# Kernel tuning notes

Measured on AMD Instinct MI355X. Metric: run time of the kernel, lower is better.

The kernel has to match this reference:

```python
import jax, jax.numpy as jnp
import numpy as np

N = 100000
E = 1600000
R = 8
DIN = 128
H = 128
C = 16
NROOT = 1024


def rgcn_conv(x, src, dst, edge_type, w_rel, w_root, bias):
    """PyG RGCNConv: per-relation mean aggregation + root weight + bias."""
    n, din = x.shape
    r = w_rel.shape[0]
    msgs = x[src]  # [E, din] gather
    seg = dst * r + edge_type  # combined (node, relation) segment id
    sums = jax.ops.segment_sum(msgs, seg, num_segments=n * r)        # [N*R, din]
    cnt = jax.ops.segment_sum(jnp.ones((msgs.shape[0],), x.dtype), seg,
                              num_segments=n * r)                    # [N*R]
    mean = sums / jnp.maximum(cnt, 1.0)[:, None]
    mean = mean.reshape(n, r, din)
    # relation-specific transform then sum over relations, plus root transform
    out = jnp.einsum('nrd,rde->ne', mean, w_rel) + x @ w_root + bias
    return out


def setup_inputs() -> dict:
    key = jax.random.key(0)
    ks = jax.random.split(key, 16)
    s = 0.05
    return {
        'x': jax.random.normal(ks[0], (N, DIN), jnp.float32),
        'edge_index': jax.random.randint(ks[1], (2, E), 0, N, jnp.int64),
        'edge_type': jax.random.randint(ks[2], (E,), 0, R, jnp.int64),
        'root_idx': jax.random.randint(ks[3], (NROOT,), 0, N, jnp.int64),
        'wrel1': jax.random.normal(ks[4], (R, DIN, H), jnp.float32) * s,
        'root1': jax.random.normal(ks[5], (DIN, H), jnp.float32) * s,
        'b1': jax.random.normal(ks[6], (H,), jnp.float32) * s,
        'wrel2': jax.random.normal(ks[7], (R, H, H), jnp.float32) * s,
        'root2': jax.random.normal(ks[8], (H, H), jnp.float32) * s,
        'b2': jax.random.normal(ks[9], (H,), jnp.float32) * s,
        'wrel3': jax.random.normal(ks[10], (R, H, C), jnp.float32) * s,
        'root3': jax.random.normal(ks[11], (H, C), jnp.float32) * s,
        'b3': jax.random.normal(ks[12], (C,), jnp.float32) * s,
    }


def reference(x, edge_index, edge_type, root_idx,
              wrel1, root1, b1, wrel2, root2, b2, wrel3, root3, b3):
    src, dst = edge_index[0], edge_index[1]
    h = jax.nn.relu(rgcn_conv(x, src, dst, edge_type, wrel1, root1, b1))
    # hidden conv (relu; dropout is identity in eval mode)
    h = jax.nn.relu(rgcn_conv(h, src, dst, edge_type, wrel2, root2, b2))
    # final conv, no activation
    h = rgcn_conv(h, src, dst, edge_type, wrel3, root3, b3)
    return h[root_idx]  # [NROOT, C]
```

## Files before the change

kernel.cpp:

```cpp
#include <hip/hip_runtime.h>
#include <hip/hip_fp16.h>


typedef _Float16 f16;
typedef _Float16 f16x2 __attribute__((ext_vector_type(2)));
typedef _Float16 f16x4 __attribute__((ext_vector_type(4)));
typedef _Float16 f16x8 __attribute__((ext_vector_type(8)));
typedef float f32x4 __attribute__((ext_vector_type(4)));

#define NREL 8
#define ACHUNK 8192

__global__ void k_hist(const int* __restrict__ dst, int E, int* __restrict__ cnt) {
  int e = blockIdx.x * 256 + threadIdx.x;
  if (e < E) atomicAdd(&cnt[dst[e]], 1);
}

__global__ void k_scan1(const int* __restrict__ in, int* __restrict__ out,
                        int* __restrict__ part, int n) {
  __shared__ int sh[256];
  int b = blockIdx.x, t = threadIdx.x;
  int base = b * 4096 + t * 16;
  int v[16]; int s = 0;
#pragma unroll
  for (int j = 0; j < 16; j++) { int idx = base + j; int x = (idx < n) ? in[idx] : 0; v[j] = s; s += x; }
  sh[t] = s; __syncthreads();
  for (int off = 1; off < 256; off <<= 1) {
    int x = 0; if (t >= off) x = sh[t - off];
    __syncthreads();
    if (t >= off) sh[t] += x;
    __syncthreads();
  }
  int excl = (t == 0) ? 0 : sh[t - 1];
  if (t == 255) part[b] = sh[255];
#pragma unroll
  for (int j = 0; j < 16; j++) { int idx = base + j; if (idx < n) out[idx] = v[j] + excl; }
}

__global__ void k_scan2(int* __restrict__ part, int nb) {
  __shared__ int sh[256];
  int t = threadIdx.x;
  sh[t] = (t < nb) ? part[t] : 0; __syncthreads();
  for (int off = 1; off < 256; off <<= 1) {
    int x = 0; if (t >= off) x = sh[t - off];
    __syncthreads();
    if (t >= off) sh[t] += x;
    __syncthreads();
  }
  if (t < nb) part[t] = (t == 0) ? 0 : sh[t - 1];
}

__global__ void k_scan3(int* __restrict__ out, const int* __restrict__ part, int n) {
  int i = blockIdx.x * 256 + threadIdx.x;
  if (i < n) out[i] += part[i >> 12];
}

__global__ void k_scatter(const int* __restrict__ src, const int* __restrict__ dstv,
                          const int* __restrict__ et, int E,
                          const int* __restrict__ off, int* __restrict__ fill,
                          int* __restrict__ sps) {
  int e = blockIdx.x * 256 + threadIdx.x;
  if (e >= E) return;
  int d = dstv[e];
  int pos = off[d] + atomicAdd(&fill[d], 1);
  sps[pos] = src[e] | (et[e] << 20);
}

__global__ void k_sentinel(int* __restrict__ p, int v) { *p = v; }

__global__ __launch_bounds__(256) void k_bhist(const int* __restrict__ dstv, int E,
                                               int* __restrict__ bcnt, int nbuck) {
  __shared__ int h[512];
  int t = threadIdx.x;
  for (int i = t; i < 512; i += 256) h[i] = 0;
  __syncthreads();
  int lo = blockIdx.x * ACHUNK;
  int hi = lo + ACHUNK < E ? lo + ACHUNK : E;
  for (int e = lo + t; e < hi; e += 256) atomicAdd(&h[dstv[e] >> 8], 1);
  __syncthreads();
  for (int i = t; i < nbuck; i += 256)
    if (h[i]) atomicAdd(&bcnt[i], h[i]);
}

__global__ __launch_bounds__(512) void k_bscan(const int* __restrict__ bcnt,
                                               int* __restrict__ boff, int nbuck) {
  __shared__ int sh[512];
  int t = threadIdx.x;
  sh[t] = (t < nbuck) ? bcnt[t] : 0;
  __syncthreads();
  for (int o = 1; o < 512; o <<= 1) {
    int v = 0; if (t >= o) v = sh[t - o];
    __syncthreads();
    sh[t] += v;
    __syncthreads();
  }
  if (t <= nbuck && t < 512) boff[t] = (t == 0) ? 0 : sh[t - 1];
  if (t == 511 && nbuck >= 512) boff[nbuck] = sh[511];
}

__global__ __launch_bounds__(256) void k_bucketA(
    const int* __restrict__ src, const int* __restrict__ dstv,
    const int* __restrict__ et, int E, const int* __restrict__ boff,
    int* __restrict__ bfill, int* __restrict__ tmp, int nbuck) {
  __shared__ int hist[512];
  __shared__ int base[512];
  int t = threadIdx.x;
  int lo = blockIdx.x * ACHUNK;
  int hi = lo + ACHUNK < E ? lo + ACHUNK : E;
  for (int i = t; i < nbuck; i += 256) hist[i] = 0;
  __syncthreads();
  for (int e = lo + t; e < hi; e += 256)
    atomicAdd(&hist[dstv[e] >> 8], 1);
  __syncthreads();
  for (int i = t; i < nbuck; i += 256) {
    int c = hist[i];
    base[i] = c ? (boff[i] + atomicAdd(&bfill[i], c)) : 0;
  }
  __syncthreads();
  for (int e = lo + t; e < hi; e += 256) {
    int d = dstv[e];
    int b = d >> 8;
    int pos = atomicAdd(&base[b], 1);
    tmp[pos] = src[e] | (et[e] << 20) | ((d & 255) << 23);
  }
}

__global__ __launch_bounds__(256) void k_bucketB2(const int* __restrict__ tmp,
                                                  const int* __restrict__ boff,
                                                  int* __restrict__ off,
                                                  int* __restrict__ sps, int N) {
  __shared__ int cnt[256];
  __shared__ int sh[256];
  __shared__ int loff[257];
  int b = blockIdx.x, t = threadIdx.x;
  int n0 = b << 8;
  int nn = (N - n0) < 256 ? (N - n0) : 256;
  cnt[t] = 0;
  __syncthreads();
  int e0 = boff[b], e1 = boff[b + 1];
  for (int e = e0 + t; e < e1; e += 256)
    atomicAdd(&cnt[(tmp[e] >> 23) & 255], 1);
  __syncthreads();
  sh[t] = cnt[t];
  __syncthreads();
  for (int o = 1; o < 256; o <<= 1) {
    int v = 0; if (t >= o) v = sh[t - o];
    __syncthreads();
    sh[t] += v;
    __syncthreads();
  }
  loff[t] = (t == 0) ? 0 : sh[t - 1];
  if (t == 255) loff[256] = sh[255];
  __syncthreads();
  if (t < nn) off[n0 + t] = e0 + loff[t];
  cnt[t] = 0;
  __syncthreads();
  for (int e = e0 + t; e < e1; e += 256) {
    int v = tmp[e];
    int dl = (v >> 23) & 255;
    int pos = e0 + loff[dl] + atomicAdd(&cnt[dl], 1);
    sps[pos] = v & 0x7FFFFF;
  }
}

__global__ void k_mark(const int* __restrict__ ridx, const int* __restrict__ off,
                       const int* __restrict__ sps, int* __restrict__ mark) {
  int i = blockIdx.x, t = threadIdx.x;
  int n = ridx[i];
  if (t == 0) mark[n] = 1;
  int e0 = off[n], e1 = off[n + 1];
  for (int e = e0 + t; e < e1; e += 64) mark[sps[e] & 0xFFFFF] = 1;
}

__global__ __launch_bounds__(256) void k_sinvp(const int* __restrict__ sps,
                                               const int* __restrict__ off,
                                               float* __restrict__ sinvp, int N) {
  __shared__ int c[16][8];
  int t = threadIdx.x;
  int g = t >> 4, st = t & 15;
  int n = blockIdx.x * 16 + g;
  if (st < 8) c[g][st] = 0;
  __syncthreads();
  if (n < N) {
    int e0 = off[n], e1 = off[n + 1];
    for (int e = e0 + st; e < e1; e += 16)
      atomicAdd(&c[g][((unsigned)sps[e]) >> 20], 1);
  }
  __syncthreads();
  if (n < N && st < 8) {
    int cc = c[g][st];
    sinvp[n * 8 + st] = 1.0f / (float)(cc > 1 ? cc : 1);
  }
}

__global__ void k_f32_to_f16(const float* __restrict__ in, f16* __restrict__ out, int n4) {
  int i = blockIdx.x * 256 + threadIdx.x;
  if (i < n4) {
    float4 v = ((const float4*)in)[i];
    f16x4 o; o[0] = (f16)v.x; o[1] = (f16)v.y; o[2] = (f16)v.z; o[3] = (f16)v.w;
    ((f16x4*)out)[i] = o;
  }
}

__global__ void k_tpw(const float* __restrict__ wrel, const float* __restrict__ wroot,
                      f16* __restrict__ dst, int PW, int p) {
  int row = blockIdx.x, k = threadIdx.x;
  float v = 0.f;
  if (row < 9 * PW) {
    int cb = row / PW, j = row - cb * PW;
    int col = p * PW + j;
    v = (cb < 8) ? wrel[(size_t)cb * 16384 + k * 128 + col] : wroot[k * 128 + col];
  }
  dst[(size_t)row * 128 + k] = (f16)v;
}

__global__ __launch_bounds__(256) void k_gemm3(const f16* __restrict__ A,
                                               const f16* __restrict__ Bt,
                                               f16* __restrict__ Y, int M, int ncol) {
  __shared__ f16 As[128 * 136];
  int tid = threadIdx.x;
  int m0 = blockIdx.x * 128;
  int PW = ncol / 9;
  int cbs = (PW == 64) ? 6 : 5;
#pragma unroll
  for (int cch = 0; cch < 8; cch++) {
    int ci = tid + cch * 256;
    int row = ci >> 4, c8 = ci & 15;
    int gm = m0 + row;
    f16x8 va = {};
    if (gm < M) va = *(const f16x8*)(A + (size_t)gm * 128 + c8 * 8);
    *(f16x8*)(As + row * 136 + c8 * 8) = va;
  }
  __syncthreads();
  int wid = tid >> 6, lane = tid & 63;
  int wm = (wid & 1) * 64, wn = (wid >> 1) * 64;
  int lm = lane & 15, lk = lane >> 4;
  f16x8 af[4][4];
#pragma unroll
  for (int ks = 0; ks < 4; ks++)
#pragma unroll
    for (int i = 0; i < 4; i++)
      af[ks][i] = *(const f16x8*)(As + (wm + i * 16 + lm) * 136 + ks * 32 + lk * 8);
  __syncthreads();
  f16* H = As;
  int NT = (ncol + 127) >> 7;
  for (int nt = blockIdx.y; nt < NT; nt += gridDim.y) {
    int n0 = nt * 128;
    f32x4 acc[4][4] = {};
#pragma unroll
    for (int ks = 0; ks < 4; ks++) {
      f16x8 b[4];
#pragma unroll
      for (int j = 0; j < 4; j++)
        b[j] = *(const f16x8*)(Bt + (size_t)(n0 + wn + j * 16 + lm) * 128 + ks * 32 + lk * 8);
#pragma unroll
      for (int i = 0; i < 4; i++)
#pragma unroll
        for (int j = 0; j < 4; j++)
          acc[i][j] = __builtin_amdgcn_mfma_f32_16x16x32_f16(b[j], af[ks][i], acc[i][j], 0, 0, 0);
    }
#pragma unroll
    for (int i = 0; i < 4; i++)
#pragma unroll
      for (int j = 0; j < 4; j++) {
        f16x4 o;
        o[0] = (f16)acc[i][j][0]; o[1] = (f16)acc[i][j][1];
        o[2] = (f16)acc[i][j][2]; o[3] = (f16)acc[i][j][3];
        *(f16x4*)(H + (wm + i * 16 + lm) * 136 + wn + j * 16 + lk * 4) = o;
      }
    __syncthreads();
    for (int i = tid; i < 128 * 16; i += 256) {
      int row = i >> 4, c8 = i & 15;
      int gm = m0 + row;
      int gc = n0 + c8 * 8;
      if (gm < M && gc < ncol) {
        int cb = gc >> cbs, wi = gc & (PW - 1);
        *(f16x8*)(Y + ((size_t)cb * M + gm) * PW + wi) =
            *(const f16x8*)(H + row * 136 + c8 * 8);
      }
    }
    __syncthreads();
  }
}

template <int PW>
__global__ __launch_bounds__(256) void k_edge_v(
    const f16* __restrict__ Y, const int* __restrict__ sps,
    const int* __restrict__ off, const float* __restrict__ sinvp,
    const float* __restrict__ bias, f16* __restrict__ hout,
    const int* __restrict__ mark, int N, int pass) {
  constexpr int CPL = PW / 16;
  int t = threadIdx.x;
  int g = t >> 4, st = t & 15;
  int n = blockIdx.x * 16 + g;
  if (n >= N) return;
  if (mark && !mark[n]) return;
  float sv = (st < 8) ? sinvp[n * 8 + st] : 0.f;
  int e0 = off[n], e1 = off[n + 1];
  float a[CPL], b2[CPL];
  {
    const f16* rp = Y + ((size_t)8 * N + n) * PW + st * CPL;
    const float* bp = bias + pass * PW + st * CPL;
#pragma unroll
    for (int q = 0; q < CPL; q++) { a[q] = (float)rp[q] + bp[q]; b2[q] = 0.f; }
  }
  int sgbase = t & 48;
  int e = e0;
  for (; e + 1 < e1; e += 2) {
    int p0 = sps[e], p1 = sps[e + 1];
    int s0 = p0 & 0xFFFFF, ty0 = ((unsigned)p0) >> 20;
    int s1 = p1 & 0xFFFFF, ty1 = ((unsigned)p1) >> 20;
    float sc0 = __shfl(sv, sgbase | ty0);
    float sc1 = __shfl(sv, sgbase | ty1);
    const f16* q0 = Y + ((size_t)ty0 * N + s0) * PW + st * CPL;
    const f16* q1 = Y + ((size_t)ty1 * N + s1) * PW + st * CPL;
    if constexpr (PW == 64) {
      f16x4 v0 = *(const f16x4*)q0;
      f16x4 v1 = *(const f16x4*)q1;
      a[0] += (float)v0[0] * sc0; a[1] += (float)v0[1] * sc0;
      a[2] += (float)v0[2] * sc0; a[3] += (float)v0[3] * sc0;
      b2[0] += (float)v1[0] * sc1; b2[1] += (float)v1[1] * sc1;
      b2[2] += (float)v1[2] * sc1; b2[3] += (float)v1[3] * sc1;
    } else {
      f16x2 v0 = *(const f16x2*)q0;
      f16x2 v1 = *(const f16x2*)q1;
      a[0] += (float)v0[0] * sc0; a[1] += (float)v0[1] * sc0;
      b2[0] += (float)v1[0] * sc1; b2[1] += (float)v1[1] * sc1;
    }
  }
  if (e < e1) {
    int p0 = sps[e];
    int s0 = p0 & 0xFFFFF, ty0 = ((unsigned)p0) >> 20;
    float sc0 = __shfl(sv, sgbase | ty0);
    const f16* q0 = Y + ((size_t)ty0 * N + s0) * PW + st * CPL;
    if constexpr (PW == 64) {
      f16x4 v0 = *(const f16x4*)q0;
      a[0] += (float)v0[0] * sc0; a[1] += (float)v0[1] * sc0;
      a[2] += (float)v0[2] * sc0; a[3] += (float)v0[3] * sc0;
    } else {
      f16x2 v0 = *(const f16x2*)q0;
      a[0] += (float)v0[0] * sc0; a[1] += (float)v0[1] * sc0;
    }
  }
  if constexpr (PW == 64) {
    f16x4 o;
#pragma unroll
    for (int q = 0; q < 4; q++) o[q] = (f16)fmaxf(a[q] + b2[q], 0.f);
    *(f16x4*)(hout + (size_t)n * 128 + pass * PW + st * 4) = o;
  } else {
    f16x2 o;
#pragma unroll
    for (int q = 0; q < 2; q++) o[q] = (f16)fmaxf(a[q] + b2[q], 0.f);
    *(f16x2*)(hout + (size_t)n * 128 + pass * PW + st * 2) = o;
  }
}

__global__ __launch_bounds__(128) void k_layer3(const f16* __restrict__ h2,
                                                const int* __restrict__ sps,
                                                const int* __restrict__ off,
                                                const float* __restrict__ sinvp,
                                                const int* __restrict__ ridx,
                                                const float* __restrict__ wrel,
                                                const float* __restrict__ wroot,
                                                const float* __restrict__ b3,
                                                float* __restrict__ out) {
  __shared__ f16 W[9 * 2048];
  __shared__ float red[2][16];
  __shared__ float sinv_s[8];
  int t = threadIdx.x;
  int n = ridx[blockIdx.x];
  for (int j = t; j < 9 * 2048; j += 128)
    W[j] = (f16)((j < 8 * 2048) ? wrel[j] : wroot[j - 8 * 2048]);
  if (t < 8) sinv_s[t] = sinvp[n * 8 + t];
  __syncthreads();
  int e0 = off[n], e1 = off[n + 1];
  int c = t & 15, kg = t >> 4;
  float a = 0.f;
  for (int e = e0; e < e1; e++) {
    int ps = sps[e];
    int s = ps & 0xFFFFF, ty = ((unsigned)ps) >> 20;
    float p = 0.f;
#pragma unroll
    for (int j = 0; j < 16; j++) {
      int k = kg * 16 + j;
      p += (float)h2[(size_t)s * 128 + k] * (float)W[ty * 2048 + k * 16 + c];
    }
    a += sinv_s[ty] * p;
  }
  {
    float p = 0.f;
#pragma unroll
    for (int j = 0; j < 16; j++) {
      int k = kg * 16 + j;
      p += (float)h2[(size_t)n * 128 + k] * (float)W[8 * 2048 + k * 16 + c];
    }
    a += p;
  }
  a += __shfl_xor(a, 16);
  a += __shfl_xor(a, 32);
  if ((t & 63) < 16) red[t >> 6][t & 15] = a;
  __syncthreads();
  if (t < 16) out[(size_t)blockIdx.x * 16 + t] = red[0][t] + red[1][t] + b3[t];
}

extern "C" void kernel_launch(void* const* d_in, const int* in_sizes, int n_in,
                              void* d_out, int out_size, void* d_ws, size_t ws_size,
                              hipStream_t stream) {
  const float* x     = (const float*)d_in[0];
  const int*   eidx  = (const int*)d_in[1];
  const int*   etyp  = (const int*)d_in[2];
  const int*   ridx  = (const int*)d_in[3];
  const float* wrel1 = (const float*)d_in[4];
  const float* root1 = (const float*)d_in[5];
  const float* b1    = (const float*)d_in[6];
  const float* wrel2 = (const float*)d_in[7];
  const float* root2 = (const float*)d_in[8];
  const float* b2    = (const float*)d_in[9];
  const float* wrel3 = (const float*)d_in[10];
  const float* root3 = (const float*)d_in[11];
  const float* b3    = (const float*)d_in[12];

  int N = in_sizes[0] / 128;
  int E = in_sizes[2];
  int NROOT = in_sizes[3];
  const int* esrc = eidx;
  const int* edst = eidx + E;

  char* p = (char*)d_ws;
  auto alloc = [&](size_t bytes) { void* r = (void*)p; p += (bytes + 255) & ~(size_t)255; return r; };
  int*   off   = (int*)alloc((size_t)(N + 1) * 4);
  int*   sps   = (int*)alloc((size_t)E * 4);
  f16*   h1    = (f16*)alloc((size_t)N * 128 * 2);
  f16*   h2    = (f16*)alloc((size_t)N * 128 * 2);
  int*   mark  = (int*)alloc((size_t)N * 4);
  float* sinvp = (float*)alloc((size_t)N * 8 * 4);
  f16*   Wt    = (f16*)alloc((size_t)640 * 128 * 2);
  int*   bcnt  = (int*)alloc(512 * 4);
  int*   boff  = (int*)alloc(513 * 4);
  int*   bfill = (int*)alloc(512 * 4);

  size_t used = (size_t)(p - (char*)d_ws);
  size_t remain = ws_size > used ? ws_size - used : 0;
  int PW = (remain >= (size_t)N * 9 * 64 * 2 + (1u << 20)) ? 64 : 32;
  int ldy = 9 * PW;
  f16* Y = (f16*)alloc((size_t)N * ldy * 2);
  int* tmp  = (int*)Y;
  int* part = tmp + E;
  int* fill = part + 4096;

  int nbuck = (N + 255) >> 8;
  int nbA = (E + ACHUNK - 1) / ACHUNK;
  hipMemsetAsync(mark, 0, (size_t)N * 4, stream);

  if (nbuck <= 512) {
    hipMemsetAsync(bcnt, 0, 512 * 4, stream);
    hipMemsetAsync(bfill, 0, 512 * 4, stream);
    k_bhist<<<nbA, 256, 0, stream>>>(edst, E, bcnt, nbuck);
    k_bscan<<<1, 512, 0, stream>>>(bcnt, boff, nbuck);
    k_bucketA<<<nbA, 256, 0, stream>>>(esrc, edst, etyp, E, boff, bfill, tmp, nbuck);
    k_bucketB2<<<nbuck, 256, 0, stream>>>(tmp, boff, off, sps, N);
    k_sentinel<<<1, 1, 0, stream>>>(off + N, E);
  } else {
    int eb = (E + 255) / 256;
    hipMemsetAsync(off, 0, (size_t)(N + 1) * 4, stream);
    hipMemsetAsync(fill, 0, (size_t)N * 4, stream);
    k_hist<<<eb, 256, 0, stream>>>(edst, E, off);
    int nb1 = (N + 4095) / 4096;
    k_scan1<<<nb1, 256, 0, stream>>>(off, off, part, N);
    k_scan2<<<1, 256, 0, stream>>>(part, nb1);
    k_scan3<<<(N + 255) / 256, 256, 0, stream>>>(off, part, N);
    k_sentinel<<<1, 1, 0, stream>>>(off + N, E);
    k_scatter<<<eb, 256, 0, stream>>>(esrc, edst, etyp, E, off, fill, sps);
  }
  k_mark<<<NROOT, 64, 0, stream>>>(ridx, off, sps, mark);
  int ng16 = (N + 15) / 16;
  k_sinvp<<<ng16, 256, 0, stream>>>(sps, off, sinvp, N);
  k_f32_to_f16<<<((N * 32) + 255) / 256, 256, 0, stream>>>(x, h2, N * 32);

  int mb = (N + 127) / 128;
  int NT = (ldy + 127) / 128;
  int npass = 128 / PW;

  for (int ps = 0; ps < npass; ps++) {
    k_tpw<<<NT * 128, 128, 0, stream>>>(wrel1, root1, Wt, PW, ps);
    k_gemm3<<<dim3(mb, 2), 256, 0, stream>>>(h2, Wt, Y, N, ldy);
    if (PW == 64)
      k_edge_v<64><<<ng16, 256, 0, stream>>>(Y, sps, off, sinvp, b1, h1, nullptr, N, ps);
    else
      k_edge_v<32><<<ng16, 256, 0, stream>>>(Y, sps, off, sinvp, b1, h1, nullptr, N, ps);
  }
  for (int ps = 0; ps < npass; ps++) {
    k_tpw<<<NT * 128, 128, 0, stream>>>(wrel2, root2, Wt, PW, ps);
    k_gemm3<<<dim3(mb, 2), 256, 0, stream>>>(h1, Wt, Y, N, ldy);
    if (PW == 64)
      k_edge_v<64><<<ng16, 256, 0, stream>>>(Y, sps, off, sinvp, b2, h2, mark, N, ps);
    else
      k_edge_v<32><<<ng16, 256, 0, stream>>>(Y, sps, off, sinvp, b2, h2, mark, N, ps);
  }
  k_layer3<<<NROOT, 128, 0, stream>>>(h2, sps, off, sinvp, ridx, wrel3, root3, b3,
                                      (float*)d_out);
}
```

Measured before the change: 500.8 us.

## Fuse sinvp into bucket sort, convert x inside GEMM, batch weight transposes

Per-(node,relation) counts are now gathered in the bucket-sort second pass, so the inverse counts come from that pass and the separate k_sinvp sweep over sps is dropped on the main path. The first-layer GEMM reads fp32 x directly and converts it to fp16 while loading to shared memory, which removes the standalone f32-to-f16 kernel and its extra write and read of the feature matrix. All weight transposes for both layers and every pass are done in one launch at the start, which removes the per-pass k_tpw launches. In exchange the bucket kernel uses more shared memory and the first GEMM reads twice as many bytes of A.

Result: faster. 476.0 us (-4.9%).

```diff
diff --git a/kernel.cpp b/kernel.cpp
--- a/kernel.cpp
+++ b/kernel.cpp
@@ -10,6 +10,7 @@
 
 #define NREL 8
 #define ACHUNK 8192
+#define WTELEM (640 * 128)
 
 __global__ void k_hist(const int* __restrict__ dst, int E, int* __restrict__ cnt) {
   int e = blockIdx.x * 256 + threadIdx.x;
@@ -66,6 +67,27 @@
   sps[pos] = src[e] | (et[e] << 20);
 }
 
+__global__ __launch_bounds__(256) void k_sinvp(const int* __restrict__ sps,
+                                               const int* __restrict__ off,
+                                               float* __restrict__ sinvp, int N) {
+  __shared__ int c[16][8];
+  int t = threadIdx.x;
+  int g = t >> 4, st = t & 15;
+  int n = blockIdx.x * 16 + g;
+  if (st < 8) c[g][st] = 0;
+  __syncthreads();
+  if (n < N) {
+    int e0 = off[n], e1 = off[n + 1];
+    for (int e = e0 + st; e < e1; e += 16)
+      atomicAdd(&c[g][((unsigned)sps[e]) >> 20], 1);
+  }
+  __syncthreads();
+  if (n < N && st < 8) {
+    int cc = c[g][st];
+    sinvp[n * 8 + st] = 1.0f / (float)(cc > 1 ? cc : 1);
+  }
+}
+
 __global__ void k_sentinel(int* __restrict__ p, int v) { *p = v; }
 
 __global__ __launch_bounds__(256) void k_bhist(const int* __restrict__ dstv, int E,
@@ -125,23 +147,34 @@
   }
 }
 
-__global__ __launch_bounds__(256) void k_bucketB2(const int* __restrict__ tmp,
+__global__ __launch_bounds__(256) void k_bucketB3(const int* __restrict__ tmp,
                                                   const int* __restrict__ boff,
                                                   int* __restrict__ off,
-                                                  int* __restrict__ sps, int N) {
-  __shared__ int cnt[256];
+                                                  int* __restrict__ sps,
+                                                  float* __restrict__ sinvp, int N) {
+  __shared__ int cty[2048];
   __shared__ int sh[256];
   __shared__ int loff[257];
+  __shared__ int fill[256];
   int b = blockIdx.x, t = threadIdx.x;
   int n0 = b << 8;
   int nn = (N - n0) < 256 ? (N - n0) : 256;
-  cnt[t] = 0;
+#pragma unroll
+  for (int j = 0; j < 8; j++) cty[t + j * 256] = 0;
   __syncthreads();
   int e0 = boff[b], e1 = boff[b + 1];
-  for (int e = e0 + t; e < e1; e += 256)
-    atomicAdd(&cnt[(tmp[e] >> 23) & 255], 1);
-  __syncthreads();
-  sh[t] = cnt[t];
+  for (int e = e0 + t; e < e1; e += 256) {
+    int v = tmp[e];
+    int dl = (v >> 23) & 255, ty = (v >> 20) & 7;
+    atomicAdd(&cty[dl * 8 + ty], 1);
+  }
+  __syncthreads();
+  {
+    int c = 0;
+#pragma unroll
+    for (int j = 0; j < 8; j++) c += cty[t * 8 + j];
+    sh[t] = c;
+  }
   __syncthreads();
   for (int o = 1; o < 256; o <<= 1) {
     int v = 0; if (t >= o) v = sh[t - o];
@@ -153,12 +186,19 @@
   if (t == 255) loff[256] = sh[255];
   __syncthreads();
   if (t < nn) off[n0 + t] = e0 + loff[t];
-  cnt[t] = 0;
+  for (int i = t; i < 2048; i += 256) {
+    int n = n0 + (i >> 3);
+    if (n < N) {
+      int c = cty[i];
+      sinvp[(size_t)n * 8 + (i & 7)] = 1.0f / (float)(c > 1 ? c : 1);
+    }
+  }
+  fill[t] = 0;
   __syncthreads();
   for (int e = e0 + t; e < e1; e += 256) {
     int v = tmp[e];
     int dl = (v >> 23) & 255;
-    int pos = e0 + loff[dl] + atomicAdd(&cnt[dl], 1);
+    int pos = e0 + loff[dl] + atomicAdd(&fill[dl], 1);
     sps[pos] = v & 0x7FFFFF;
   }
 }
@@ -172,49 +212,24 @@
   for (int e = e0 + t; e < e1; e += 64) mark[sps[e] & 0xFFFFF] = 1;
 }
 
-__global__ __launch_bounds__(256) void k_sinvp(const int* __restrict__ sps,
-                                               const int* __restrict__ off,
-                                               float* __restrict__ sinvp, int N) {
-  __shared__ int c[16][8];
-  int t = threadIdx.x;
-  int g = t >> 4, st = t & 15;
-  int n = blockIdx.x * 16 + g;
-  if (st < 8) c[g][st] = 0;
-  __syncthreads();
-  if (n < N) {
-    int e0 = off[n], e1 = off[n + 1];
-    for (int e = e0 + st; e < e1; e += 16)
-      atomicAdd(&c[g][((unsigned)sps[e]) >> 20], 1);
-  }
-  __syncthreads();
-  if (n < N && st < 8) {
-    int cc = c[g][st];
-    sinvp[n * 8 + st] = 1.0f / (float)(cc > 1 ? cc : 1);
-  }
-}
-
-__global__ void k_f32_to_f16(const float* __restrict__ in, f16* __restrict__ out, int n4) {
-  int i = blockIdx.x * 256 + threadIdx.x;
-  if (i < n4) {
-    float4 v = ((const float4*)in)[i];
-    f16x4 o; o[0] = (f16)v.x; o[1] = (f16)v.y; o[2] = (f16)v.z; o[3] = (f16)v.w;
-    ((f16x4*)out)[i] = o;
-  }
-}
-
-__global__ void k_tpw(const float* __restrict__ wrel, const float* __restrict__ wroot,
-                      f16* __restrict__ dst, int PW, int p) {
-  int row = blockIdx.x, k = threadIdx.x;
+__global__ void k_tpw4(const float* __restrict__ wrel1, const float* __restrict__ root1,
+                       const float* __restrict__ wrel2, const float* __restrict__ root2,
+                       f16* __restrict__ Wt, int PW, int npass) {
+  int row = blockIdx.x, k = threadIdx.x, q = blockIdx.y;
+  int layer = q / npass, p = q - layer * npass;
+  const float* wrel = layer ? wrel2 : wrel1;
+  const float* wroot = layer ? root2 : root1;
   float v = 0.f;
   if (row < 9 * PW) {
     int cb = row / PW, j = row - cb * PW;
     int col = p * PW + j;
     v = (cb < 8) ? wrel[(size_t)cb * 16384 + k * 128 + col] : wroot[k * 128 + col];
   }
-  dst[(size_t)row * 128 + k] = (f16)v;
-}
-
-__global__ __launch_bounds__(256) void k_gemm3(const f16* __restrict__ A,
+  Wt[(size_t)q * WTELEM + (size_t)row * 128 + k] = (f16)v;
+}
+
+template <typename AT>
+__global__ __launch_bounds__(256) void k_gemm3(const AT* __restrict__ A,
                                                const f16* __restrict__ Bt,
                                                f16* __restrict__ Y, int M, int ncol) {
   __shared__ f16 As[128 * 136];
@@ -228,7 +243,16 @@
     int row = ci >> 4, c8 = ci & 15;
     int gm = m0 + row;
     f16x8 va = {};
-    if (gm < M) va = *(const f16x8*)(A + (size_t)gm * 128 + c8 * 8);
+    if (gm < M) {
+      if constexpr (sizeof(AT) == 2) {
+        va = *(const f16x8*)((const f16*)A + (size_t)gm * 128 + c8 * 8);
+      } else {
+        const float4* ap = (const float4*)((const float*)A + (size_t)gm * 128);
+        float4 u0 = ap[c8 * 2], u1 = ap[c8 * 2 + 1];
+        va[0] = (f16)u0.x; va[1] = (f16)u0.y; va[2] = (f16)u0.z; va[3] = (f16)u0.w;
+        va[4] = (f16)u1.x; va[5] = (f16)u1.y; va[6] = (f16)u1.z; va[7] = (f16)u1.w;
+      }
+    }
     *(f16x8*)(As + row * 136 + c8 * 8) = va;
   }
   __syncthreads();
@@ -434,7 +458,7 @@
   f16*   h2    = (f16*)alloc((size_t)N * 128 * 2);
   int*   mark  = (int*)alloc((size_t)N * 4);
   float* sinvp = (float*)alloc((size_t)N * 8 * 4);
-  f16*   Wt    = (f16*)alloc((size_t)640 * 128 * 2);
+  f16*   Wt    = (f16*)alloc((size_t)WTELEM * 2 * 8);
   int*   bcnt  = (int*)alloc(512 * 4);
   int*   boff  = (int*)alloc(513 * 4);
   int*   bfill = (int*)alloc(512 * 4);
@@ -450,7 +474,11 @@
 
   int nbuck = (N + 255) >> 8;
   int nbA = (E + ACHUNK - 1) / ACHUNK;
+  int npass = 128 / PW;
+  int NT = (ldy + 127) / 128;
   hipMemsetAsync(mark, 0, (size_t)N * 4, stream);
+  k_tpw4<<<dim3(NT * 128, 2 * npass), 128, 0, stream>>>(wrel1, root1, wrel2, root2,
+                                                        Wt, PW, npass);
 
   if (nbuck <= 512) {
     hipMemsetAsync(bcnt, 0, 512 * 4, stream);
@@ -458,7 +486,7 @@
     k_bhist<<<nbA, 256, 0, stream>>>(edst, E, bcnt, nbuck);
     k_bscan<<<1, 512, 0, stream>>>(bcnt, boff, nbuck);
     k_bucketA<<<nbA, 256, 0, stream>>>(esrc, edst, etyp, E, boff, bfill, tmp, nbuck);
-    k_bucketB2<<<nbuck, 256, 0, stream>>>(tmp, boff, off, sps, N);
+    k_bucketB3<<<nbuck, 256, 0, stream>>>(tmp, boff, off, sps, sinvp, N);
     k_sentinel<<<1, 1, 0, stream>>>(off + N, E);
   } else {
     int eb = (E + 255) / 256;
@@ -471,27 +499,24 @@
     k_scan3<<<(N + 255) / 256, 256, 0, stream>>>(off, part, N);
     k_sentinel<<<1, 1, 0, stream>>>(off + N, E);
     k_scatter<<<eb, 256, 0, stream>>>(esrc, edst, etyp, E, off, fill, sps);
+    int ng16f = (N + 15) / 16;
+    k_sinvp<<<ng16f, 256, 0, stream>>>(sps, off, sinvp, N);
   }
   k_mark<<<NROOT, 64, 0, stream>>>(ridx, off, sps, mark);
   int ng16 = (N + 15) / 16;
-  k_sinvp<<<ng16, 256, 0, stream>>>(sps, off, sinvp, N);
-  k_f32_to_f16<<<((N * 32) + 255) / 256, 256, 0, stream>>>(x, h2, N * 32);
 
   int mb = (N + 127) / 128;
-  int NT = (ldy + 127) / 128;
-  int npass = 128 / PW;
 
   for (int ps = 0; ps < npass; ps++) {
-    k_tpw<<<NT * 128, 128, 0, stream>>>(wrel1, root1, Wt, PW, ps);
-    k_gemm3<<<dim3(mb, 2), 256, 0, stream>>>(h2, Wt, Y, N, ldy);
+    k_gemm3<float><<<dim3(mb, 2), 256, 0, stream>>>(x, Wt + (size_t)ps * WTELEM, Y, N, ldy);
     if (PW == 64)
       k_edge_v<64><<<ng16, 256, 0, stream>>>(Y, sps, off, sinvp, b1, h1, nullptr, N, ps);
     else
       k_edge_v<32><<<ng16, 256, 0, stream>>>(Y, sps, off, sinvp, b1, h1, nullptr, N, ps);
   }
   for (int ps = 0; ps < npass; ps++) {
-    k_tpw<<<NT * 128, 128, 0, stream>>>(wrel2, root2, Wt, PW, ps);
-    k_gemm3<<<dim3(mb, 2), 256, 0, stream>>>(h1, Wt, Y, N, ldy);
+    k_gemm3<f16><<<dim3(mb, 2), 256, 0, stream>>>(h1, Wt + (size_t)(npass + ps) * WTELEM,
+                                                  Y, N, ldy);
     if (PW == 64)
       k_edge_v<64><<<ng16, 256, 0, stream>>>(Y, sps, off, sinvp, b2, h2, mark, N, ps);
     else
```
